# Optimization experiments

Measured on AMD Instinct MI355X. Metric: run time of the kernel, lower is better.

## Reference

```python
import jax, jax.numpy as jnp
import numpy as np

NUM_HEADS = 16

def setup_inputs() -> dict:
    key = jax.random.key(0)
    k1, k2, k3 = jax.random.split(key, 3)
    T, B, E = 2048, 4, 1024
    x = jax.random.normal(k1, (T, B, E), dtype=jnp.float32)
    # xavier-ish scaled weights
    in_proj_w = jax.random.normal(k2, (3 * E, E), dtype=jnp.float32) * (1.0 / np.sqrt(E))
    in_proj_b = jnp.zeros((3 * E,), dtype=jnp.float32)
    out_w = jax.random.normal(k3, (E, E), dtype=jnp.float32) * (1.0 / np.sqrt(E))
    out_b = jnp.zeros((E,), dtype=jnp.float32)
    return {"x": x, "in_proj_w": in_proj_w, "in_proj_b": in_proj_b,
            "out_w": out_w, "out_b": out_b}

def reference(x, in_proj_w, in_proj_b, out_w, out_b):
    # Self-attention (query=key=value=x), shapes: x [T, B, E]
    T, B, E = x.shape
    H = NUM_HEADS
    D = E // H
    scaling = D ** -0.5
    # fused QKV projection: [T, B, 3E]
    qkv = jnp.einsum('tbe,fe->tbf', x, in_proj_w) + in_proj_b
    q, k, v = jnp.split(qkv, 3, axis=-1)
    q = q * scaling
    # [T, B, E] -> [B, H, T, D]
    def to_heads(t):
        return t.reshape(T, B, H, D).transpose(1, 2, 0, 3)
    q, k, v = to_heads(q), to_heads(k), to_heads(v)
    # scores [B, H, T, T], softmax in float32 as in the original
    scores = jnp.einsum('bhtd,bhsd->bhts', q, k)
    attn_weights = jax.nn.softmax(scores.astype(jnp.float32), axis=-1).astype(scores.dtype)
    # attn [B, H, T, D] -> [T, B, E]
    attn = jnp.einsum('bhts,bhsd->bhtd', attn_weights, v)
    attn = attn.transpose(2, 0, 1, 3).reshape(T, B, E)
    out = jnp.einsum('tbe,fe->tbf', attn, out_w) + out_b
    # averaged attention weights over heads: [B, T, T]
    avg_weights = attn_weights.sum(axis=1) / H
    return out, avg_weights
```

## Files before the change

kernel.cpp:

```cpp
#include <hip/hip_runtime.h>
#include <hip/hip_bf16.h>
#include <cstdint>
#include <cstddef>

typedef __attribute__((ext_vector_type(8))) short s16x8;
typedef __attribute__((ext_vector_type(4))) float f32x4;
typedef __attribute__((ext_vector_type(8))) _Float16 h8;
typedef __attribute__((ext_vector_type(4))) _Float16 h4;

#define TT 2048
#define BB 4
#define EE 1024
#define HH 16
#define DD 64
#define MR 8192

#define MFMA_BF16(a,b,c) __builtin_amdgcn_mfma_f32_16x16x32_bf16(a,b,c,0,0,0)
#define MFMA_F16(a,b,c)  __builtin_amdgcn_mfma_f32_16x16x32_f16(a,b,c,0,0,0)

__device__ __forceinline__ ushort f2bf(float f) {
  uint32_t u = __float_as_uint(f);
  u += 0x7fffu + ((u >> 16) & 1u);
  return (ushort)(u >> 16);
}

#define GL2L(g, l) __builtin_amdgcn_global_load_lds( \
    (__attribute__((address_space(1))) void*)(g), \
    (__attribute__((address_space(3))) void*)(l), 16, 0, 0)

__global__ void cast_f32_bf16(const float* __restrict__ in, ushort* __restrict__ out, int n4) {
  int stride = gridDim.x * blockDim.x;
  for (int i = blockIdx.x * blockDim.x + threadIdx.x; i < n4; i += stride) {
    float4 v = ((const float4*)in)[i];
    ushort4 o;
    o.x = f2bf(v.x); o.y = f2bf(v.y); o.z = f2bf(v.z); o.w = f2bf(v.w);
    ((ushort4*)out)[i] = o;
  }
}

__global__ __launch_bounds__(256) void gemm_qkv(
    const ushort* __restrict__ A, const ushort* __restrict__ W,
    const float* __restrict__ bias,
    ushort* __restrict__ Qb, ushort* __restrict__ Kb, ushort* __restrict__ Vt)
{
  __shared__ ushort As[128 * 32];
  __shared__ ushort Bs[128 * 32];
  const int K = EE;
  int tid = threadIdx.x;
  int bn = blockIdx.x, bm = blockIdx.y;
  int brow = bm * 128, bcol = bn * 128;
  int lane = tid & 63, wid = tid >> 6;
  int wm = wid >> 1, wn = wid & 1;
  int lr = lane & 15, kg = lane >> 4;

  f32x4 zero = {0.f, 0.f, 0.f, 0.f};
  f32x4 acc[4][4];
#pragma unroll
  for (int i = 0; i < 4; i++)
#pragma unroll
    for (int j = 0; j < 4; j++) acc[i][j] = zero;

  int r0 = tid >> 2, c0 = (tid & 3) * 8;
  const ushort* Abase = A + (size_t)brow * K;
  const ushort* Wbase = W + (size_t)bcol * K;

  for (int k0 = 0; k0 < K; k0 += 32) {
    __syncthreads();
    GL2L(Abase + (size_t)r0 * K + k0 + c0,        &As[tid * 8]);
    GL2L(Abase + (size_t)(r0 + 64) * K + k0 + c0, &As[(tid + 256) * 8]);
    GL2L(Wbase + (size_t)r0 * K + k0 + c0,        &Bs[tid * 8]);
    GL2L(Wbase + (size_t)(r0 + 64) * K + k0 + c0, &Bs[(tid + 256) * 8]);
    __syncthreads();
    s16x8 af[4], bfr[4];
#pragma unroll
    for (int i = 0; i < 4; i++) af[i]  = *(const s16x8*)&As[(wm * 64 + i * 16 + lr) * 32 + kg * 8];
#pragma unroll
    for (int j = 0; j < 4; j++) bfr[j] = *(const s16x8*)&Bs[(wn * 64 + j * 16 + lr) * 32 + kg * 8];
#pragma unroll
    for (int i = 0; i < 4; i++)
#pragma unroll
      for (int j = 0; j < 4; j++)
        acc[i][j] = MFMA_BF16(af[i], bfr[j], acc[i][j]);
  }

#pragma unroll
  for (int i = 0; i < 4; i++)
#pragma unroll
    for (int j = 0; j < 4; j++) {
      int n = bcol + wn * 64 + j * 16 + lr;
      float bv = bias[n];
      int sec = n >> 10;
      int hd = n & 1023;
      int h = hd >> 6, d = hd & 63;
#pragma unroll
      for (int e = 0; e < 4; e++) {
        int m = brow + wm * 64 + i * 16 + kg * 4 + e;
        int t = m >> 2, b = m & 3;
        float v = acc[i][j][e] + bv;
        size_t hoff = (size_t)(b * HH + h);
        if (sec == 0)      Qb[(hoff * TT + t) * DD + d] = f2bf(v * 0.180336880f);
        else if (sec == 1) Kb[(hoff * TT + t) * DD + d] = f2bf(v);
        else { _Float16 hv = (_Float16)v; Vt[(hoff * DD + d) * TT + t] = *(ushort*)&hv; }
      }
    }
}

__global__ __launch_bounds__(512) void attn_fused(
    const ushort* __restrict__ Qb, const ushort* __restrict__ Kb,
    const _Float16* __restrict__ Vt, ushort* __restrict__ attn,
    float* __restrict__ avgp)
{
  __shared__ _Float16 sc[32 * 2048];
  __shared__ float scr[2048];
  __shared__ float pmax[32][8];
  __shared__ float invl[32];

  const int qt = blockIdx.x;
  const int b  = blockIdx.y;
  const int tid = threadIdx.x;
  const int lane = tid & 63;
  const int w = tid >> 6;
  const int m = lane & 15;
  const int kq = lane >> 4;
  const int t0 = qt * 32;

  h8 av[4][4];
#pragma unroll
  for (int u = 0; u < 4; u++)
#pragma unroll
    for (int c = 0; c < 4; c++)
#pragma unroll
      for (int j = 0; j < 8; j++) av[u][c][j] = (_Float16)0.f;

  for (int h = 0; h < HH; ++h) {
    const size_t bh = (size_t)b * HH + h;

    const ushort* qp = Qb + (bh * TT + t0) * DD;
    s16x8 q00 = *(const s16x8*)&qp[(size_t)m * DD + kq * 8];
    s16x8 q01 = *(const s16x8*)&qp[(size_t)m * DD + 32 + kq * 8];
    s16x8 q10 = *(const s16x8*)&qp[(size_t)(16 + m) * DD + kq * 8];
    s16x8 q11 = *(const s16x8*)&qp[(size_t)(16 + m) * DD + 32 + kq * 8];

    const ushort* kbase = Kb + bh * TT * DD;
    float mx0 = -3e38f, mx1 = -3e38f;
#pragma unroll 4
    for (int i = 0; i < 16; ++i) {
      int nt = w * 16 + i;
      const ushort* kr = kbase + (size_t)(nt * 16 + m) * DD + kq * 8;
      s16x8 a0 = *(const s16x8*)kr;
      s16x8 a1 = *(const s16x8*)(kr + 32);
      f32x4 c0 = {0.f, 0.f, 0.f, 0.f}, c1 = {0.f, 0.f, 0.f, 0.f};
      c0 = MFMA_BF16(a0, q00, c0); c0 = MFMA_BF16(a1, q01, c0);
      c1 = MFMA_BF16(a0, q10, c1); c1 = MFMA_BF16(a1, q11, c1);
      int ksw = (nt * 16 + kq * 4) ^ ((m & 7) << 3);
      h4 p0, p1;
#pragma unroll
      for (int e = 0; e < 4; e++) {
        mx0 = fmaxf(mx0, c0[e]); mx1 = fmaxf(mx1, c1[e]);
        p0[e] = (_Float16)c0[e]; p1[e] = (_Float16)c1[e];
      }
      *(h4*)&sc[(size_t)m * 2048 + ksw] = p0;
      *(h4*)&sc[(size_t)(16 + m) * 2048 + ksw] = p1;
    }
    mx0 = fmaxf(mx0, __shfl_xor(mx0, 16)); mx0 = fmaxf(mx0, __shfl_xor(mx0, 32));
    mx1 = fmaxf(mx1, __shfl_xor(mx1, 16)); mx1 = fmaxf(mx1, __shfl_xor(mx1, 32));
    if (lane < 16) { pmax[m][w] = mx0; pmax[16 + m][w] = mx1; }
    __syncthreads();

#pragma unroll
    for (int u = 0; u < 4; ++u) {
      int r = w * 4 + u;
      _Float16* rp = &sc[(size_t)r * 2048];
      int xr = (r & 7) << 3;
      float mx = -3e38f;
#pragma unroll
      for (int j = 0; j < 8; ++j) mx = fmaxf(mx, pmax[r][j]);
      f32x4 lv0 = {0.f, 0.f, 0.f, 0.f};
      f32x4 lv1 = {0.f, 0.f, 0.f, 0.f};
      h8 eh[4];
#pragma unroll
      for (int c = 0; c < 4; ++c) {
        h8 t = *(const h8*)&rp[((c * 64 + lane) * 8) ^ xr];
        h8 e;
#pragma unroll
        for (int j = 0; j < 4; j++) { float ef = exp2f((float)t[j] - mx); lv0[j] += ef; e[j] = (_Float16)ef; }
#pragma unroll
        for (int j = 4; j < 8; j++) { float ef = exp2f((float)t[j] - mx); lv1[j - 4] += ef; e[j] = (_Float16)ef; }
        *(h8*)&rp[((c * 64 + lane) * 8) ^ xr] = e;
        eh[c] = e;
      }
      float l = ((lv0[0] + lv0[1]) + (lv0[2] + lv0[3]))
              + ((lv1[0] + lv1[1]) + (lv1[2] + lv1[3]));
#pragma unroll
      for (int o = 32; o; o >>= 1) l += __shfl_xor(l, o);
      float inv = 1.0f / l;
      if (lane == 0) invl[r] = inv;
      _Float16 hinv = (_Float16)inv;
#pragma unroll
      for (int c = 0; c < 4; ++c)
#pragma unroll
        for (int j = 0; j < 8; j++)
          av[u][c][j] += eh[c][j] * hinv;
    }
    __syncthreads();

    {
      int dtl = w & 3, kh = w >> 2;
      const _Float16* vb = Vt + bh * DD * TT + (size_t)(dtl * 16 + m) * TT + kh * 1024 + kq * 8;
      const _Float16* a0p = &sc[(size_t)m * 2048];
      const _Float16* a1p = &sc[(size_t)(16 + m) * 2048];
      int xr = (m & 7) << 3;
      f32x4 accA0 = {0.f, 0.f, 0.f, 0.f}, accB0 = {0.f, 0.f, 0.f, 0.f};
      f32x4 accA1 = {0.f, 0.f, 0.f, 0.f}, accB1 = {0.f, 0.f, 0.f, 0.f};
#pragma unroll 2
      for (int s = 0; s < 32; s += 2) {
        int ksw0 = (kh * 1024 + s * 32 + kq * 8) ^ xr;
        int ksw1 = (kh * 1024 + (s + 1) * 32 + kq * 8) ^ xr;
        h8 bv0 = *(const h8*)(vb + s * 32);
        h8 bv1 = *(const h8*)(vb + (s + 1) * 32);
        h8 a00 = *(const h8*)&a0p[ksw0];
        h8 a01 = *(const h8*)&a0p[ksw1];
        h8 a10 = *(const h8*)&a1p[ksw0];
        h8 a11 = *(const h8*)&a1p[ksw1];
        accA0 = MFMA_F16(a00, bv0, accA0);
        accB0 = MFMA_F16(a01, bv1, accB0);
        accA1 = MFMA_F16(a10, bv0, accA1);
        accB1 = MFMA_F16(a11, bv1, accB1);
      }
      if (kh == 1) {
#pragma unroll
        for (int e = 0; e < 4; e++) {
          scr[(dtl * 2 + 0) * 256 + (kq * 4 + e) * 16 + m] = accA0[e] + accB0[e];
          scr[(dtl * 2 + 1) * 256 + (kq * 4 + e) * 16 + m] = accA1[e] + accB1[e];
        }
      }
      __syncthreads();
      if (kh == 0) {
#pragma unroll
        for (int e = 0; e < 4; e++) {
          int ql = kq * 4 + e;
          float v0 = (accA0[e] + accB0[e] + scr[(dtl * 2 + 0) * 256 + ql * 16 + m]) * invl[ql];
          float v1 = (accA1[e] + accB1[e] + scr[(dtl * 2 + 1) * 256 + ql * 16 + m]) * invl[16 + ql];
          attn[((size_t)(t0 + ql) * BB + b) * EE + h * DD + dtl * 16 + m] = f2bf(v0);
          attn[((size_t)(t0 + 16 + ql) * BB + b) * EE + h * DD + dtl * 16 + m] = f2bf(v1);
        }
      }
    }
    __syncthreads();
  }

#pragma unroll
  for (int u = 0; u < 4; ++u) {
    float* gp = avgp + ((size_t)b * TT + t0 + w * 4 + u) * TT;
#pragma unroll
    for (int c = 0; c < 4; ++c) {
      int cb = (c * 64 + lane) * 8;
      float4 o0 = {(float)av[u][c][0] * 0.0625f, (float)av[u][c][1] * 0.0625f,
                   (float)av[u][c][2] * 0.0625f, (float)av[u][c][3] * 0.0625f};
      float4 o1 = {(float)av[u][c][4] * 0.0625f, (float)av[u][c][5] * 0.0625f,
                   (float)av[u][c][6] * 0.0625f, (float)av[u][c][7] * 0.0625f};
      ((float4*)(gp + cb))[0] = o0;
      ((float4*)(gp + cb))[1] = o1;
    }
  }
}

__global__ __launch_bounds__(256) void gemm_out(
    const ushort* __restrict__ A, const ushort* __restrict__ W,
    const float* __restrict__ bias, float* __restrict__ out)
{
  __shared__ ushort As[128 * 32];
  __shared__ ushort Bs[128 * 32];
  const int K = EE;
  int tid = threadIdx.x;
  int bn = blockIdx.x, bm = blockIdx.y;
  int brow = bm * 128, bcol = bn * 128;
  int lane = tid & 63, wid = tid >> 6;
  int wm = wid >> 1, wn = wid & 1;
  int lr = lane & 15, kg = lane >> 4;

  f32x4 zero = {0.f, 0.f, 0.f, 0.f};
  f32x4 acc[4][4];
#pragma unroll
  for (int i = 0; i < 4; i++)
#pragma unroll
    for (int j = 0; j < 4; j++) acc[i][j] = zero;

  int r0 = tid >> 2, c0 = (tid & 3) * 8;
  const ushort* Abase = A + (size_t)brow * K;
  const ushort* Wbase = W + (size_t)bcol * K;

  for (int k0 = 0; k0 < K; k0 += 32) {
    __syncthreads();
    GL2L(Abase + (size_t)r0 * K + k0 + c0,        &As[tid * 8]);
    GL2L(Abase + (size_t)(r0 + 64) * K + k0 + c0, &As[(tid + 256) * 8]);
    GL2L(Wbase + (size_t)r0 * K + k0 + c0,        &Bs[tid * 8]);
    GL2L(Wbase + (size_t)(r0 + 64) * K + k0 + c0, &Bs[(tid + 256) * 8]);
    __syncthreads();
    s16x8 af[4], bfr[4];
#pragma unroll
    for (int i = 0; i < 4; i++) af[i]  = *(const s16x8*)&As[(wm * 64 + i * 16 + lr) * 32 + kg * 8];
#pragma unroll
    for (int j = 0; j < 4; j++) bfr[j] = *(const s16x8*)&Bs[(wn * 64 + j * 16 + lr) * 32 + kg * 8];
#pragma unroll
    for (int i = 0; i < 4; i++)
#pragma unroll
      for (int j = 0; j < 4; j++)
        acc[i][j] = MFMA_BF16(af[i], bfr[j], acc[i][j]);
  }

#pragma unroll
  for (int i = 0; i < 4; i++)
#pragma unroll
    for (int j = 0; j < 4; j++) {
      int n = bcol + wn * 64 + j * 16 + lr;
      float bv = bias[n];
#pragma unroll
      for (int e = 0; e < 4; e++) {
        int m = brow + wm * 64 + i * 16 + kg * 4 + e;
        out[(size_t)m * EE + n] = acc[i][j][e] + bv;
      }
    }
}

extern "C" void kernel_launch(void* const* d_in, const int* in_sizes, int n_in,
                              void* d_out, int out_size, void* d_ws, size_t ws_size,
                              hipStream_t stream) {
  const float* x  = (const float*)d_in[0];
  const float* w1 = (const float*)d_in[1];
  const float* b1 = (const float*)d_in[2];
  const float* w2 = (const float*)d_in[3];
  const float* b2 = (const float*)d_in[4];
  float* out = (float*)d_out;
  float* avg = out + (size_t)MR * EE;

  char* p = (char*)d_ws;
  ushort* Xb   = (ushort*)p; p += (size_t)MR * EE * 2;
  ushort* W1b  = (ushort*)p; p += (size_t)3 * EE * EE * 2;
  ushort* W2b  = (ushort*)p; p += (size_t)EE * EE * 2;
  ushort* Qb   = (ushort*)p; p += (size_t)BB * HH * TT * DD * 2;
  ushort* Kb   = (ushort*)p; p += (size_t)BB * HH * TT * DD * 2;
  ushort* Vt   = (ushort*)p; p += (size_t)BB * HH * TT * DD * 2;
  ushort* attn = (ushort*)p; p += (size_t)MR * EE * 2;
  (void)ws_size;

  cast_f32_bf16<<<1024, 256, 0, stream>>>(x,  Xb,  MR * EE / 4);
  cast_f32_bf16<<<512,  256, 0, stream>>>(w1, W1b, 3 * EE * EE / 4);
  cast_f32_bf16<<<256,  256, 0, stream>>>(w2, W2b, EE * EE / 4);
  gemm_qkv<<<dim3(24, 64), 256, 0, stream>>>(Xb, W1b, b1, Qb, Kb, Vt);
  attn_fused<<<dim3(TT / 32, BB), 512, 0, stream>>>(Qb, Kb, (const _Float16*)Vt, attn, avg);
  gemm_out<<<dim3(8, 64), 256, 0, stream>>>(attn, W2b, b2, out);
}
```

Baseline: 486.3 us.

## Split PV matmul across waves by key range and reduce partials through shared memory

The P·V stage now gives each of the 8 waves a 256-key slice and all 4 D-tiles, instead of 4 D-tiles times 2 key halves. Each wave loads its A fragments from the score buffer once and reuses them across 4 D-tiles. The 8 partial accumulators are written into the reused score buffer and reduced cooperatively, which drops the separate scratch array and lets the output be stored as vectorized 4-element bf16 writes. In exchange there is an 8-way shared-memory reduction, more accumulator registers, and V loads strided across 4 rows per step.

```diff
diff --git a/kernel.cpp b/kernel.cpp
--- a/kernel.cpp
+++ b/kernel.cpp
@@ -110,8 +110,7 @@
     const _Float16* __restrict__ Vt, ushort* __restrict__ attn,
     float* __restrict__ avgp)
 {
-  __shared__ _Float16 sc[32 * 2048];
-  __shared__ float scr[2048];
+  __shared__ __align__(16) _Float16 sc[32 * 2048];
   __shared__ float pmax[32][8];
   __shared__ float invl[32];
 
@@ -123,6 +122,10 @@
   const int m = lane & 15;
   const int kq = lane >> 4;
   const int t0 = qt * 32;
+
+  const int rsb = tid >> 6;
+  const int rqi = tid & 15;
+  const int rd0 = ((tid >> 4) & 3) * 4;
 
   h8 av[4][4];
 #pragma unroll
@@ -205,45 +208,50 @@
     __syncthreads();
 
     {
-      int dtl = w & 3, kh = w >> 2;
-      const _Float16* vb = Vt + bh * DD * TT + (size_t)(dtl * 16 + m) * TT + kh * 1024 + kq * 8;
-      const _Float16* a0p = &sc[(size_t)m * 2048];
-      const _Float16* a1p = &sc[(size_t)(16 + m) * 2048];
+      const _Float16* ap0 = &sc[(size_t)m * 2048];
+      const _Float16* ap1 = &sc[(size_t)(16 + m) * 2048];
+      const _Float16* vbh = Vt + bh * DD * TT;
       int xr = (m & 7) << 3;
-      f32x4 accA0 = {0.f, 0.f, 0.f, 0.f}, accB0 = {0.f, 0.f, 0.f, 0.f};
-      f32x4 accA1 = {0.f, 0.f, 0.f, 0.f}, accB1 = {0.f, 0.f, 0.f, 0.f};
-#pragma unroll 2
-      for (int s = 0; s < 32; s += 2) {
-        int ksw0 = (kh * 1024 + s * 32 + kq * 8) ^ xr;
-        int ksw1 = (kh * 1024 + (s + 1) * 32 + kq * 8) ^ xr;
-        h8 bv0 = *(const h8*)(vb + s * 32);
-        h8 bv1 = *(const h8*)(vb + (s + 1) * 32);
-        h8 a00 = *(const h8*)&a0p[ksw0];
-        h8 a01 = *(const h8*)&a0p[ksw1];
-        h8 a10 = *(const h8*)&a1p[ksw0];
-        h8 a11 = *(const h8*)&a1p[ksw1];
-        accA0 = MFMA_F16(a00, bv0, accA0);
-        accB0 = MFMA_F16(a01, bv1, accB0);
-        accA1 = MFMA_F16(a10, bv0, accA1);
-        accB1 = MFMA_F16(a11, bv1, accB1);
-      }
-      if (kh == 1) {
-#pragma unroll
-        for (int e = 0; e < 4; e++) {
-          scr[(dtl * 2 + 0) * 256 + (kq * 4 + e) * 16 + m] = accA0[e] + accB0[e];
-          scr[(dtl * 2 + 1) * 256 + (kq * 4 + e) * 16 + m] = accA1[e] + accB1[e];
+      f32x4 acc[2][4];
+#pragma unroll
+      for (int rg = 0; rg < 2; ++rg)
+#pragma unroll
+        for (int dtl = 0; dtl < 4; ++dtl) acc[rg][dtl] = (f32x4){0.f, 0.f, 0.f, 0.f};
+#pragma unroll 4
+      for (int s = 0; s < 8; ++s) {
+        int kb2 = w * 256 + s * 32 + kq * 8;
+        int ksw = kb2 ^ xr;
+        h8 a0 = *(const h8*)&ap0[ksw];
+        h8 a1 = *(const h8*)&ap1[ksw];
+#pragma unroll
+        for (int dtl = 0; dtl < 4; ++dtl) {
+          h8 bv = *(const h8*)(vbh + (size_t)(dtl * 16 + m) * TT + kb2);
+          acc[0][dtl] = MFMA_F16(a0, bv, acc[0][dtl]);
+          acc[1][dtl] = MFMA_F16(a1, bv, acc[1][dtl]);
         }
       }
       __syncthreads();
-      if (kh == 0) {
-#pragma unroll
-        for (int e = 0; e < 4; e++) {
-          int ql = kq * 4 + e;
-          float v0 = (accA0[e] + accB0[e] + scr[(dtl * 2 + 0) * 256 + ql * 16 + m]) * invl[ql];
-          float v1 = (accA1[e] + accB1[e] + scr[(dtl * 2 + 1) * 256 + ql * 16 + m]) * invl[16 + ql];
-          attn[((size_t)(t0 + ql) * BB + b) * EE + h * DD + dtl * 16 + m] = f2bf(v0);
-          attn[((size_t)(t0 + 16 + ql) * BB + b) * EE + h * DD + dtl * 16 + m] = f2bf(v1);
+      float* pb = (float*)sc;
+#pragma unroll
+      for (int rg = 0; rg < 2; ++rg)
+#pragma unroll
+        for (int dtl = 0; dtl < 4; ++dtl)
+          *(f32x4*)&pb[(size_t)((w * 8 + rg * 4 + dtl) * 256) + m * 16 + kq * 4] = acc[rg][dtl];
+      __syncthreads();
+      {
+        f32x4 sum = {0.f, 0.f, 0.f, 0.f};
+#pragma unroll
+        for (int wv = 0; wv < 8; ++wv) {
+          const float* sp = &pb[(size_t)((wv * 8 + rsb) * 256)];
+#pragma unroll
+          for (int e = 0; e < 4; ++e) sum[e] += sp[(rd0 + e) * 16 + rqi];
         }
+        int rg = rsb >> 2, dtl = rsb & 3;
+        float inv = invl[rg * 16 + rqi];
+        ushort4 o;
+        o.x = f2bf(sum[0] * inv); o.y = f2bf(sum[1] * inv);
+        o.z = f2bf(sum[2] * inv); o.w = f2bf(sum[3] * inv);
+        *(ushort4*)&attn[((size_t)(t0 + rg * 16 + rqi) * BB + b) * EE + h * DD + dtl * 16 + rd0] = o;
       }
     }
     __syncthreads();
```

New measurement: 529.8 us. +9.0%, slower.
